# Kernel tuning notes

Measured on AMD Instinct MI355X. Metric: run time of the kernel, lower is better.

Reference implementation:

```python
import jax, jax.numpy as jnp
import numpy as np

EMBED_DIM = 1024
NUM_HEAD = 16
HEAD_DIM = EMBED_DIM // NUM_HEAD
B, T = 4, 2048


def setup_inputs() -> dict:
    key = jax.random.key(0)
    ks = jax.random.split(key, 6)
    s_in = 1.0 / np.sqrt(EMBED_DIM)
    return {
        "hidden_states": jax.random.normal(ks[0], (B, T, EMBED_DIM), dtype=jnp.float32),
        "attn_mask": jnp.ones((B, T), dtype=jnp.int32),
        "W_qkv": jax.random.uniform(ks[1], (3 * EMBED_DIM, EMBED_DIM), jnp.float32, -s_in, s_in),
        "b_qkv": jax.random.uniform(ks[2], (3 * EMBED_DIM,), jnp.float32, -s_in, s_in),
        "W_o": jax.random.uniform(ks[3], (EMBED_DIM, EMBED_DIM), jnp.float32, -s_in, s_in),
        "b_o": jax.random.uniform(ks[4], (EMBED_DIM,), jnp.float32, -s_in, s_in),
    }


def reference(hidden_states, attn_mask, W_qkv, b_qkv, W_o, b_o):
    Bb, Tt, C = hidden_states.shape
    H, D = NUM_HEAD, HEAD_DIM
    scaling = D ** (-0.5)

    qkv = hidden_states @ W_qkv.T + b_qkv  # [B,T,3C]
    q, k, v = jnp.split(qkv, 3, axis=-1)
    # [B,H,T,D]
    q = q.reshape(Bb, Tt, H, D).transpose(0, 2, 1, 3)
    k = k.reshape(Bb, Tt, H, D).transpose(0, 2, 1, 3)
    v = v.reshape(Bb, Tt, H, D).transpose(0, 2, 1, 3)

    scores = jnp.einsum("bhqd,bhkd->bhqk", q, k) * scaling  # [B,H,T,T]

    causal = jnp.tril(jnp.ones((Tt, Tt), dtype=bool))[None, None]  # [1,1,T,T]
    am = attn_mask.astype(bool)
    mask = causal & am[:, None, :, None] & am[:, None, None, :]  # [B,1,T,T]
    scores = jnp.where(mask, scores, -jnp.inf)

    probs = jax.nn.softmax(scores, axis=-1)
    out = jnp.einsum("bhqk,bhkd->bhqd", probs, v)  # [B,H,T,D]
    out = out.transpose(0, 2, 1, 3).reshape(Bb, Tt, C)
    return out @ W_o.T + b_o
```

## Files before the change

kernel.cpp:

```cpp
#include <hip/hip_runtime.h>
#include <cstdint>
#include <cstddef>
#include <math.h>

#define BATCH 4
#define TSEQ  2048
#define CDIM  1024
#define NH    16
#define HDIM  64
#define MTOT  (BATCH * TSEQ)


typedef __attribute__((ext_vector_type(4))) float  floatx4;
typedef __attribute__((ext_vector_type(8))) short  shortx8;
typedef __attribute__((ext_vector_type(4))) short  shortx4;

__device__ __forceinline__ short f2bf(float f) {
    union { float f; unsigned int u; } v; v.f = f;
    unsigned int lsb = (v.u >> 16) & 1u;
    v.u += 0x7fffu + lsb;
    return (short)(v.u >> 16);
}

#if defined(__has_builtin)
#  if __has_builtin(__builtin_amdgcn_exp2f)
#    define EXP2F(x) __builtin_amdgcn_exp2f(x)
#  else
#    define EXP2F(x) exp2f(x)
#  endif
#  if __has_builtin(__builtin_amdgcn_perm)
__device__ __forceinline__ unsigned pack_hi16(unsigned hi, unsigned lo) {
    return __builtin_amdgcn_perm(hi, lo, 0x07060302u);
}
#  else
__device__ __forceinline__ unsigned pack_hi16(unsigned hi, unsigned lo) {
    return (lo >> 16) | (hi & 0xffff0000u);
}
#  endif
#  if __has_builtin(__builtin_amdgcn_mfma_f32_16x16x16bf16_1k)
#    define HAS_MFMA_1K 1
#  else
#    define HAS_MFMA_1K 0
#  endif
#else
#  define EXP2F(x) exp2f(x)
__device__ __forceinline__ unsigned pack_hi16(unsigned hi, unsigned lo) {
    return (lo >> 16) | (hi & 0xffff0000u);
}
#  define HAS_MFMA_1K 0
#endif

#define QSCALE (0.125f * 1.44269504088896f)

__global__ __launch_bounds__(256) void cvt_kernel(const float4* __restrict__ src,
                                                  shortx4* __restrict__ dst, int n4)
{
    int i = blockIdx.x * 256 + threadIdx.x;
    if (i < n4) {
        float4 v = src[i];
        shortx4 s;
        s[0] = f2bf(v.x); s[1] = f2bf(v.y); s[2] = f2bf(v.z); s[3] = f2bf(v.w);
        dst[i] = s;
    }
}

__global__ __launch_bounds__(256) void cvt3_kernel(
    const float4* __restrict__ s1, shortx4* __restrict__ d1,
    const float4* __restrict__ s2, shortx4* __restrict__ d2,
    const float4* __restrict__ s3, shortx4* __restrict__ d3)
{
    int bid = blockIdx.x;
    const float4* s; shortx4* d; int i;
    if (bid < 8192)       { s = s1; d = d1; i = bid * 256 + threadIdx.x; }
    else if (bid < 11264) { s = s2; d = d2; i = (bid - 8192) * 256 + threadIdx.x; }
    else                  { s = s3; d = d3; i = (bid - 11264) * 256 + threadIdx.x; }
    float4 v = s[i];
    shortx4 o;
    o[0] = f2bf(v.x); o[1] = f2bf(v.y); o[2] = f2bf(v.z); o[3] = f2bf(v.w);
    d[i] = o;
}

__device__ __forceinline__ void stageA_bf16(const short* g, short* S, int row0,
                                            int K, int k0, int tid, int wave)
{
#pragma unroll
    for (int i = 0; i < 2; ++i) {
        int c = i * 256 + tid;
        int r = c >> 2, kc = c & 3;
        __builtin_amdgcn_global_load_lds(
            (__attribute__((address_space(1))) void*)(g + (size_t)(row0 + r) * K + k0 + kc * 8),
            (__attribute__((address_space(3))) void*)((char*)S + i * 4096 + wave * 1024),
            16, 0, 0);
    }
}
__device__ __forceinline__ void stageB_f32(const float* g, short* S, int row0,
                                           int K, int k0, int tid)
{
#pragma unroll
    for (int i = 0; i < 4; ++i) {
        int c = i * 256 + tid;
        int r = c >> 3, fc = c & 7;
        const float4 v = *(const float4*)(g + (size_t)(row0 + r) * K + k0 + fc * 4);
        shortx4 s4;
        s4[0] = f2bf(v.x); s4[1] = f2bf(v.y); s4[2] = f2bf(v.z); s4[3] = f2bf(v.w);
        *(shortx4*)(S + r * 32 + fc * 4) = s4;
    }
}

__device__ __forceinline__ void qkv_scatter(
    const floatx4& a, const float* bias,
    short* Qo, short* Ko, short* VTo,
    int m, int n)
{
    float bv = bias[n];
    int b = m >> 11, t0 = m & (TSEQ - 1);
    int part = n >> 10, rem = n & 1023;
    int h = rem >> 6, d = rem & 63;
    if (part == 2) {
        shortx4 st;
#pragma unroll
        for (int r = 0; r < 4; ++r) st[r] = f2bf(a[r] + bv);
        *(shortx4*)(VTo + (((size_t)(b * NH + h)) * HDIM + d) * TSEQ + t0) = st;
    } else {
        short* dst = (part == 0) ? Qo : Ko;
        float scale = (part == 0) ? QSCALE : 1.0f;
#pragma unroll
        for (int r = 0; r < 4; ++r) {
            size_t idx = (((size_t)(b * NH + h)) * TSEQ + (t0 + r)) * HDIM + d;
            dst[idx] = f2bf((a[r] + bv) * scale);
        }
    }
}

__global__ __launch_bounds__(512) void gemm_qkv_fast_kernel(
    const short* __restrict__ A,
    const short* __restrict__ W,
    const float* __restrict__ bias,
    short* __restrict__ Qo, short* __restrict__ Ko, short* __restrict__ VTo)
{
    __shared__ short lds[2 * 2 * 256 * 64];

    const int tid  = threadIdx.x;
    const int lane = tid & 63, wid = tid >> 6;
    const int quad = lane >> 4, l16 = lane & 15;
    const int wm = wid >> 2, wn = wid & 3;
    const int row0 = blockIdx.x * 256;
    const int col0 = blockIdx.y * 256;
    const int NT = CDIM / 64;

#define GQ_AS1 __attribute__((address_space(1))) void*
#define GQ_AS3 __attribute__((address_space(3))) void*
#define STAGE_HALF(gbase, grow0, panel, half, k0)                             \
    {                                                                         \
        _Pragma("unroll")                                                     \
        for (int i = 0; i < 2; ++i) {                                         \
            int idx = i * 512 + tid;                                          \
            int rr = idx >> 3, cd = idx & 7;                                  \
            int cc = cd ^ (rr & 7);                                           \
            __builtin_amdgcn_global_load_lds(                                 \
                (GQ_AS1)((gbase) + (size_t)((grow0) + (half) * 128 + rr) * CDIM + (k0) + cc * 8), \
                (GQ_AS3)((char*)(panel) + (half) * 16384 + i * 8192 + wid * 1024),                \
                16, 0, 0);                                                    \
        }                                                                     \
    }

    floatx4 acc[8][4] = {};

    {
        short* A0 = lds;
        short* B0 = lds + 16384;
        STAGE_HALF(A, row0, A0, 0, 0);
        STAGE_HALF(A, row0, A0, 1, 0);
        STAGE_HALF(W, col0, B0, 0, 0);
        STAGE_HALF(W, col0, B0, 1, 0);
    }
    __syncthreads();

    for (int t = 0; t < NT; ++t) {
        const int bsel = t & 1;
        const short* Ac = lds + bsel * 32768;
        const short* Bc = Ac + 16384;
        short* An = lds + (bsel ^ 1) * 32768;
        short* Bn = An + 16384;
        const bool st = (t + 1 < NT);
        const int k1 = (t + 1) << 6;

        shortx8 bf[4][2];
#pragma unroll
        for (int q = 0; q < 4; ++q) {
            if (q == 0) {
#pragma unroll
                for (int ni = 0; ni < 4; ++ni)
#pragma unroll
                    for (int ks = 0; ks < 2; ++ks) {
                        int col = wn * 64 + ni * 16 + l16;
                        bf[ni][ks] = *(const shortx8*)(
                            Bc + col * 64 + (((ks * 4 + quad) ^ (l16 & 7)) << 3));
                    }
            }
            shortx8 af[2][2];
#pragma unroll
            for (int j = 0; j < 2; ++j)
#pragma unroll
                for (int ks = 0; ks < 2; ++ks) {
                    int row = wm * 128 + (2 * q + j) * 16 + l16;
                    af[j][ks] = *(const shortx8*)(
                        Ac + row * 64 + (((ks * 4 + quad) ^ (l16 & 7)) << 3));
                }

            if (q == 0 && st) {
                STAGE_HALF(A, row0, An, 0, k1);
                STAGE_HALF(A, row0, An, 1, k1);
            }
            if (q == 1 && st) {
                STAGE_HALF(W, col0, Bn, 0, k1);
                STAGE_HALF(W, col0, Bn, 1, k1);
            }

            __builtin_amdgcn_s_barrier();
            __builtin_amdgcn_s_setprio(1);
#pragma unroll
            for (int j = 0; j < 2; ++j)
#pragma unroll
                for (int ni = 0; ni < 4; ++ni)
#pragma unroll
                    for (int ks = 0; ks < 2; ++ks)
                        acc[2 * q + j][ni] = __builtin_amdgcn_mfma_f32_16x16x32_bf16(
                            af[j][ks], bf[ni][ks], acc[2 * q + j][ni], 0, 0, 0);
            __builtin_amdgcn_s_setprio(0);
            if (q < 3) __builtin_amdgcn_s_barrier();
        }
        __syncthreads();
    }
#undef STAGE_HALF
#undef GQ_AS1
#undef GQ_AS3

#pragma unroll
    for (int mi = 0; mi < 8; ++mi) {
        int m = row0 + wm * 128 + mi * 16 + quad * 4;
#pragma unroll
        for (int ni = 0; ni < 4; ++ni) {
            int n = col0 + wn * 64 + ni * 16 + l16;
            qkv_scatter(acc[mi][ni], bias, Qo, Ko, VTo, m, n);
        }
    }
}

__global__ __launch_bounds__(256) void gemm_qkv_kernel(
    const short* __restrict__ A,
    const float* __restrict__ W,
    const float* __restrict__ bias,
    short* __restrict__ Qo, short* __restrict__ Ko, short* __restrict__ VTo)
{
    __shared__ short As[128 * 32];
    __shared__ short Bs[128 * 32];
    const int tid  = threadIdx.x;
    const int lane = tid & 63, wave = tid >> 6;
    const int quad = lane >> 4, l16 = lane & 15;
    const int wr = wave >> 1, wc = wave & 1;
    const int row0 = blockIdx.x * 128;
    const int col0 = blockIdx.y * 128;
    const int K = CDIM;

    floatx4 acc[4][4] = {};

    for (int k0 = 0; k0 < K; k0 += 32) {
        stageA_bf16(A, As, row0, K, k0, tid, wave);
        stageB_f32(W, Bs, col0, K, k0, tid);
        __syncthreads();

        shortx8 af[4], bfr[4];
#pragma unroll
        for (int mi = 0; mi < 4; ++mi)
            af[mi] = *(const shortx8*)(As + (wr * 64 + mi * 16 + l16) * 32 + quad * 8);
#pragma unroll
        for (int ni = 0; ni < 4; ++ni)
            bfr[ni] = *(const shortx8*)(Bs + (wc * 64 + ni * 16 + l16) * 32 + quad * 8);
#pragma unroll
        for (int mi = 0; mi < 4; ++mi)
#pragma unroll
            for (int ni = 0; ni < 4; ++ni)
                acc[mi][ni] = __builtin_amdgcn_mfma_f32_16x16x32_bf16(
                    af[mi], bfr[ni], acc[mi][ni], 0, 0, 0);
        __syncthreads();
    }
#pragma unroll
    for (int mi = 0; mi < 4; ++mi) {
        int m = row0 + wr * 64 + mi * 16 + quad * 4;
#pragma unroll
        for (int ni = 0; ni < 4; ++ni) {
            int n = col0 + wc * 64 + ni * 16 + l16;
            qkv_scatter(acc[mi][ni], bias, Qo, Ko, VTo, m, n);
        }
    }
}

__global__ __launch_bounds__(256) void attn_kernel(
    const short* __restrict__ Q,
    const short* __restrict__ Kg,
    const short* __restrict__ VT,
    const int*   __restrict__ am,
    short* __restrict__ O)
{
    __shared__ short Ks[128 * 64];
    __shared__ short Vs[64 * 128];

    const int tid  = threadIdx.x;
    const int lane = tid & 63, wave = tid >> 6;
    const int quad = lane >> 4, l16 = lane & 15;

    const int L = blockIdx.x;
    const int bh = (L & 7) + (((L >> 3) & 7) << 3);
    const int strip = 15 - (L >> 6);
    const int b = bh >> 4, h = bh & 15;

    const short* Qb = Q  + (size_t)bh * TSEQ * HDIM;
    const short* Kb = Kg + (size_t)bh * TSEQ * HDIM;
    const short* Vb = VT + (size_t)bh * HDIM * TSEQ;

    const int q0  = strip * 128;
    const int qb0 = q0 + wave * 32;
    const int qv0 = qb0 + l16;
    const int qv1 = qv0 + 16;

    shortx8 bq[2][2];
#pragma unroll
    for (int nq = 0; nq < 2; ++nq)
#pragma unroll
        for (int kk = 0; kk < 2; ++kk)
            bq[nq][kk] = *(const shortx8*)(
                Qb + (size_t)(qb0 + nq * 16 + l16) * HDIM + kk * 32 + quad * 8);

    floatx4 o[4][2] = {};
    floatx4 lacc[2] = {};

#if HAS_MFMA_1K
    const shortx4 ones4 = { (short)0x3F80, (short)0x3F80, (short)0x3F80, (short)0x3F80 };
#else
    const shortx8 ones8 = { (short)0x3F80, (short)0x3F80, (short)0x3F80, (short)0x3F80,
                            (short)0x3F80, (short)0x3F80, (short)0x3F80, (short)0x3F80 };
#endif

    const int ntiles = (q0 + 128) >> 7;
    for (int kt = 0; kt < ntiles; ++kt) {
        const int kt0 = kt << 7;
#pragma unroll
        for (int i = 0; i < 4; ++i) {
            int idx = i * 256 + tid;
            int rr = idx >> 3, cd = idx & 7;
            int cc = cd ^ (rr & 7);
            __builtin_amdgcn_global_load_lds(
                (__attribute__((address_space(1))) void*)(Kb + (size_t)(kt0 + rr) * HDIM + cc * 8),
                (__attribute__((address_space(3))) void*)((char*)Ks + i * 4096 + wave * 1024),
                16, 0, 0);
            int rrv = idx >> 4, cdv = idx & 15;
            int ccv = cdv ^ (rrv & 7);
            __builtin_amdgcn_global_load_lds(
                (__attribute__((address_space(1))) void*)(Vb + (size_t)rrv * TSEQ + kt0 + ccv * 8),
                (__attribute__((address_space(3))) void*)((char*)Vs + i * 4096 + wave * 1024),
                16, 0, 0);
        }
        int amv0 = am[b * TSEQ + kt0 + lane];
        int amv1 = am[b * TSEQ + kt0 + 64 + lane];
        __syncthreads();

#pragma unroll 1
        for (int p = 0; p < 2; ++p) {
            const int pb0 = kt0 + p * 64;
            int amv = p ? amv1 : amv0;
            bool allones = (__ballot(amv != 0) == 0xFFFFFFFFFFFFFFFFULL);

            floatx4 s[4][2] = {};
#pragma unroll
            for (int kk = 0; kk < 2; ++kk)
#pragma unroll
                for (int t = 0; t < 4; ++t) {
                    int rr = p * 64 + t * 16 + l16;
                    shortx8 kf = *(const shortx8*)(
                        Ks + rr * 64 + (((kk * 4 + quad) ^ (l16 & 7)) << 3));
#pragma unroll
                    for (int nq = 0; nq < 2; ++nq)
                        s[t][nq] = __builtin_amdgcn_mfma_f32_16x16x32_bf16(
                            kf, bq[nq][kk], s[t][nq], 0, 0, 0);
                }

            unsigned pk[4][2][2];
#pragma unroll
            for (int nq = 0; nq < 2; ++nq) {
                const int qv = nq ? qv1 : qv0;
#pragma unroll
                for (int t = 0; t < 4; ++t) {
                    bool diag = (pb0 + t * 16 + 15) > (qb0 + nq * 16);
                    unsigned pu[4];
#pragma unroll
                    for (int r = 0; r < 4; ++r) {
                        float pe = EXP2F(s[t][nq][r]);
                        unsigned u = __float_as_uint(pe) & 0xffff0000u;
                        if (!allones) {
                            int amr = __shfl(amv, t * 16 + quad * 4 + r);
                            u = amr ? u : 0u;
                        }
                        if (diag) {
                            int kv = pb0 + t * 16 + quad * 4 + r;
                            u = (kv <= qv) ? u : 0u;
                        }
                        pu[r] = u;
                    }
                    pk[t][nq][0] = pack_hi16(pu[1], pu[0]);
                    pk[t][nq][1] = pack_hi16(pu[3], pu[2]);
                }
            }

#if HAS_MFMA_1K
#pragma unroll
            for (int t = 0; t < 4; ++t) {
                union { unsigned u[2]; shortx4 s; } pb[2];
                pb[0].u[0] = pk[t][0][0]; pb[0].u[1] = pk[t][0][1];
                pb[1].u[0] = pk[t][1][0]; pb[1].u[1] = pk[t][1][1];
#pragma unroll
                for (int nq = 0; nq < 2; ++nq)
                    lacc[nq] = __builtin_amdgcn_mfma_f32_16x16x16bf16_1k(
                        ones4, pb[nq].s, lacc[nq], 0, 0, 0);
#pragma unroll
                for (int mi = 0; mi < 4; ++mi) {
                    int rr = mi * 16 + l16;
                    int cidx = (p * 8 + 2 * t + (quad >> 1)) ^ (l16 & 7);
                    shortx4 vf = *(const shortx4*)(Vs + rr * 128 + cidx * 8 + (quad & 1) * 4);
#pragma unroll
                    for (int nq = 0; nq < 2; ++nq)
                        o[mi][nq] = __builtin_amdgcn_mfma_f32_16x16x16bf16_1k(
                            vf, pb[nq].s, o[mi][nq], 0, 0, 0);
                }
            }
#else
#pragma unroll
            for (int kk2 = 0; kk2 < 2; ++kk2) {
                unsigned bfr[2][4];
#pragma unroll
                for (int nq = 0; nq < 2; ++nq)
#pragma unroll
                    for (int jj = 0; jj < 4; ++jj) {
                        int srclane = (((quad & 1) * 2 + (jj >> 1)) * 16 + l16) << 2;
                        int lo = __builtin_amdgcn_ds_bpermute(srclane, (int)pk[kk2 * 2][nq][jj & 1]);
                        int hi = __builtin_amdgcn_ds_bpermute(srclane, (int)pk[kk2 * 2 + 1][nq][jj & 1]);
                        bfr[nq][jj] = (quad >> 1) ? (unsigned)hi : (unsigned)lo;
                    }
                union { unsigned u[4]; shortx8 s; } pb[2];
#pragma unroll
                for (int nq = 0; nq < 2; ++nq) {
#pragma unroll
                    for (int jj = 0; jj < 4; ++jj) pb[nq].u[jj] = bfr[nq][jj];
                    lacc[nq] = __builtin_amdgcn_mfma_f32_16x16x32_bf16(
                        ones8, pb[nq].s, lacc[nq], 0, 0, 0);
                }
#pragma unroll
                for (int mi = 0; mi < 4; ++mi) {
                    int rr = mi * 16 + l16;
                    int cidx = (p * 8 + kk2 * 4 + quad) ^ (l16 & 7);
                    shortx8 vf8 = *(const shortx8*)(Vs + rr * 128 + cidx * 8);
#pragma unroll
                    for (int nq = 0; nq < 2; ++nq)
                        o[mi][nq] = __builtin_amdgcn_mfma_f32_16x16x32_bf16(
                            vf8, pb[nq].s, o[mi][nq], 0, 0, 0);
                }
            }
#endif
        }
        __syncthreads();
    }

#pragma unroll
    for (int nq = 0; nq < 2; ++nq) {
        float inv = 1.0f / lacc[nq][0];
        int q = qb0 + nq * 16 + l16;
#pragma unroll
        for (int mi = 0; mi < 4; ++mi) {
            shortx4 st;
#pragma unroll
            for (int r = 0; r < 4; ++r) st[r] = f2bf(o[mi][nq][r] * inv);
            *(shortx4*)(O + ((size_t)(b * TSEQ + q)) * CDIM + h * HDIM + mi * 16 + quad * 4) = st;
        }
    }
}

__global__ __launch_bounds__(256) void gemm_out_kernel(
    const short* __restrict__ A,
    const short* __restrict__ W,
    const float* __restrict__ bias,
    float* __restrict__ Out)
{
    __shared__ short As[128 * 32];
    __shared__ short Bs[128 * 32];
    const int tid  = threadIdx.x;
    const int lane = tid & 63, wave = tid >> 6;
    const int quad = lane >> 4, l16 = lane & 15;
    const int wr = wave >> 1, wc = wave & 1;
    const int row0 = blockIdx.x * 128;
    const int col0 = blockIdx.y * 128;
    const int K = CDIM;

    floatx4 acc[4][4] = {};

    for (int k0 = 0; k0 < K; k0 += 32) {
        stageA_bf16(A, As, row0, K, k0, tid, wave);
        stageA_bf16(W, Bs, col0, K, k0, tid, wave);
        __syncthreads();

        shortx8 af[4], bfr[4];
#pragma unroll
        for (int mi = 0; mi < 4; ++mi)
            af[mi] = *(const shortx8*)(As + (wr * 64 + mi * 16 + l16) * 32 + quad * 8);
#pragma unroll
        for (int ni = 0; ni < 4; ++ni)
            bfr[ni] = *(const shortx8*)(Bs + (wc * 64 + ni * 16 + l16) * 32 + quad * 8);
#pragma unroll
        for (int mi = 0; mi < 4; ++mi)
#pragma unroll
            for (int ni = 0; ni < 4; ++ni)
                acc[mi][ni] = __builtin_amdgcn_mfma_f32_16x16x32_bf16(
                    af[mi], bfr[ni], acc[mi][ni], 0, 0, 0);
        __syncthreads();
    }

#pragma unroll
    for (int mi = 0; mi < 4; ++mi) {
        int m = row0 + wr * 64 + mi * 16 + quad * 4;
#pragma unroll
        for (int ni = 0; ni < 4; ++ni) {
            int n = col0 + wc * 64 + ni * 16 + l16;
            float bv = bias[n];
#pragma unroll
            for (int r = 0; r < 4; ++r)
                Out[(size_t)(m + r) * CDIM + n] = acc[mi][ni][r] + bv;
        }
    }
}

extern "C" void kernel_launch(void* const* d_in, const int* in_sizes, int n_in,
                              void* d_out, int out_size, void* d_ws, size_t ws_size,
                              hipStream_t stream)
{
    const float* hs   = (const float*)d_in[0];
    const int*   am   = (const int*)d_in[1];
    const float* Wqkv = (const float*)d_in[2];
    const float* bqkv = (const float*)d_in[3];
    const float* Wo   = (const float*)d_in[4];
    const float* bo   = (const float*)d_in[5];
    float* out = (float*)d_out;

    char* ws = (char*)d_ws;
    short* slot = (short*)ws;
    short* Qw   = (short*)(ws + ((size_t)16 << 20));
    short* Kw   = (short*)(ws + ((size_t)32 << 20));
    short* VTw  = (short*)(ws + ((size_t)48 << 20));

    if (ws_size >= ((size_t)72 << 20)) {
        short* Wqkvb = (short*)(ws + ((size_t)64 << 20));
        short* Wob   = (short*)(ws + ((size_t)70 << 20));
        cvt3_kernel<<<dim3(12288), 256, 0, stream>>>(
            (const float4*)hs,   (shortx4*)slot,
            (const float4*)Wqkv, (shortx4*)Wqkvb,
            (const float4*)Wo,   (shortx4*)Wob);
        gemm_qkv_fast_kernel<<<dim3(MTOT / 256, (3 * CDIM) / 256), 512, 0, stream>>>(
            slot, Wqkvb, bqkv, Qw, Kw, VTw);
        attn_kernel<<<dim3(1024), 256, 0, stream>>>(
            Qw, Kw, VTw, am, slot);
        gemm_out_kernel<<<dim3(MTOT / 128, CDIM / 128), 256, 0, stream>>>(
            slot, Wob, bo, out);
    } else {
        cvt_kernel<<<dim3((MTOT * CDIM / 4 + 255) / 256), 256, 0, stream>>>(
            (const float4*)hs, (shortx4*)slot, MTOT * CDIM / 4);
        gemm_qkv_kernel<<<dim3(MTOT / 128, (3 * CDIM) / 128), 256, 0, stream>>>(
            slot, Wqkv, bqkv, Qw, Kw, VTw);
        attn_kernel<<<dim3(1024), 256, 0, stream>>>(
            Qw, Kw, VTw, am, slot);
        cvt_kernel<<<dim3((CDIM * CDIM / 4 + 255) / 256), 256, 0, stream>>>(
            (const float4*)Wo, (shortx4*)Kw, CDIM * CDIM / 4);
        gemm_out_kernel<<<dim3(MTOT / 128, CDIM / 128), 256, 0, stream>>>(
            slot, Kw, bo, out);
    }
}
```

Measured before the change: 267.4 us.

## Add double-buffered direct-to-LDS output projection GEMM with 256x128 tiles

Replaces the output projection GEMM with a new kernel that uses 512 threads and 256x128 tiles. Operands are staged with global_load_lds into XOR-swizzled, double-buffered LDS panels, and the next K-tile loads are interleaved with MFMA phases under raised wave priority. The aim is to hide global load latency and improve operand reuse in the final GEMM, as was already done for the QKV GEMM. The grid shrinks to 32x8 = 256 blocks, which may leave some compute units idle, and LDS use per block grows.

Result: no change. 263.6 us (-1.4%).

```diff
diff --git a/kernel.cpp b/kernel.cpp
--- a/kernel.cpp
+++ b/kernel.cpp
@@ -233,8 +233,6 @@
         __syncthreads();
     }
 #undef STAGE_HALF
-#undef GQ_AS1
-#undef GQ_AS3
 
 #pragma unroll
     for (int mi = 0; mi < 8; ++mi) {
@@ -243,6 +241,134 @@
         for (int ni = 0; ni < 4; ++ni) {
             int n = col0 + wn * 64 + ni * 16 + l16;
             qkv_scatter(acc[mi][ni], bias, Qo, Ko, VTo, m, n);
+        }
+    }
+}
+
+__global__ __launch_bounds__(512) void gemm_out_fast_kernel(
+    const short* __restrict__ A,
+    const short* __restrict__ W,
+    const float* __restrict__ bias,
+    float* __restrict__ Out)
+{
+    __shared__ short lds[2 * (256 + 128) * 64];
+
+    const int tid  = threadIdx.x;
+    const int lane = tid & 63, wid = tid >> 6;
+    const int quad = lane >> 4, l16 = lane & 15;
+    const int wm = wid >> 2, wn = wid & 3;
+    const int row0 = blockIdx.x * 256;
+    const int col0 = blockIdx.y * 128;
+    const int NT = CDIM / 64;
+
+#define STAGE_AH(panel, half, k0)                                             \
+    {                                                                         \
+        _Pragma("unroll")                                                     \
+        for (int i = 0; i < 2; ++i) {                                         \
+            int idx = i * 512 + tid;                                          \
+            int rr = idx >> 3, cd = idx & 7;                                  \
+            int cc = cd ^ (rr & 7);                                           \
+            __builtin_amdgcn_global_load_lds(                                 \
+                (GQ_AS1)(A + (size_t)(row0 + (half) * 128 + rr) * CDIM + (k0) + cc * 8),  \
+                (GQ_AS3)((char*)(panel) + (half) * 16384 + i * 8192 + wid * 1024),        \
+                16, 0, 0);                                                    \
+        }                                                                     \
+    }
+#define STAGE_B(panel, k0)                                                    \
+    {                                                                         \
+        _Pragma("unroll")                                                     \
+        for (int i = 0; i < 2; ++i) {                                         \
+            int idx = i * 512 + tid;                                          \
+            int rr = idx >> 3, cd = idx & 7;                                  \
+            int cc = cd ^ (rr & 7);                                           \
+            __builtin_amdgcn_global_load_lds(                                 \
+                (GQ_AS1)(W + (size_t)(col0 + rr) * CDIM + (k0) + cc * 8),     \
+                (GQ_AS3)((char*)(panel) + i * 8192 + wid * 1024),             \
+                16, 0, 0);                                                    \
+        }                                                                     \
+    }
+
+    floatx4 acc[8][2] = {};
+
+    {
+        short* A0 = lds;
+        short* B0 = lds + 16384;
+        STAGE_AH(A0, 0, 0);
+        STAGE_AH(A0, 1, 0);
+        STAGE_B(B0, 0);
+    }
+    __syncthreads();
+
+    for (int t = 0; t < NT; ++t) {
+        const int bsel = t & 1;
+        const short* Ac = lds + bsel * 24576;
+        const short* Bc = Ac + 16384;
+        short* An = lds + (bsel ^ 1) * 24576;
+        short* Bn = An + 16384;
+        const bool st = (t + 1 < NT);
+        const int k1 = (t + 1) << 6;
+
+        shortx8 bf[2][2];
+#pragma unroll
+        for (int q = 0; q < 4; ++q) {
+            if (q == 0) {
+#pragma unroll
+                for (int ni = 0; ni < 2; ++ni)
+#pragma unroll
+                    for (int ks = 0; ks < 2; ++ks) {
+                        int col = wn * 32 + ni * 16 + l16;
+                        bf[ni][ks] = *(const shortx8*)(
+                            Bc + col * 64 + (((ks * 4 + quad) ^ (l16 & 7)) << 3));
+                    }
+            }
+            shortx8 af[2][2];
+#pragma unroll
+            for (int j = 0; j < 2; ++j)
+#pragma unroll
+                for (int ks = 0; ks < 2; ++ks) {
+                    int row = wm * 128 + (2 * q + j) * 16 + l16;
+                    af[j][ks] = *(const shortx8*)(
+                        Ac + row * 64 + (((ks * 4 + quad) ^ (l16 & 7)) << 3));
+                }
+
+            if (q == 0 && st) {
+                STAGE_AH(An, 0, k1);
+                STAGE_AH(An, 1, k1);
+            }
+            if (q == 1 && st) {
+                STAGE_B(Bn, k1);
+            }
+
+            __builtin_amdgcn_s_barrier();
+            __builtin_amdgcn_s_setprio(1);
+#pragma unroll
+            for (int j = 0; j < 2; ++j)
+#pragma unroll
+                for (int ni = 0; ni < 2; ++ni)
+#pragma unroll
+                    for (int ks = 0; ks < 2; ++ks)
+                        acc[2 * q + j][ni] = __builtin_amdgcn_mfma_f32_16x16x32_bf16(
+                            af[j][ks], bf[ni][ks], acc[2 * q + j][ni], 0, 0, 0);
+            __builtin_amdgcn_s_setprio(0);
+            if (q < 3) __builtin_amdgcn_s_barrier();
+        }
+        __syncthreads();
+    }
+#undef STAGE_AH
+#undef STAGE_B
+#undef GQ_AS1
+#undef GQ_AS3
+
+#pragma unroll
+    for (int mi = 0; mi < 8; ++mi) {
+        int m = row0 + wm * 128 + mi * 16 + quad * 4;
+#pragma unroll
+        for (int ni = 0; ni < 2; ++ni) {
+            int n = col0 + wn * 32 + ni * 16 + l16;
+            float bv = bias[n];
+#pragma unroll
+            for (int r = 0; r < 4; ++r)
+                Out[(size_t)(m + r) * CDIM + n] = acc[mi][ni][r] + bv;
         }
     }
 }
@@ -566,7 +692,7 @@
             slot, Wqkvb, bqkv, Qw, Kw, VTw);
         attn_kernel<<<dim3(1024), 256, 0, stream>>>(
             Qw, Kw, VTw, am, slot);
-        gemm_out_kernel<<<dim3(MTOT / 128, CDIM / 128), 256, 0, stream>>>(
+        gemm_out_fast_kernel<<<dim3(MTOT / 256, CDIM / 128), 512, 0, stream>>>(
             slot, Wob, bo, out);
     } else {
         cvt_kernel<<<dim3((MTOT * CDIM / 4 + 255) / 256), 256, 0, stream>>>(
```
